# Performance work log

Measured on AMD Instinct MI355X. Metric: run time of the kernel, lower is better.

Reference implementation:

```python
import jax, jax.numpy as jnp
from jax import lax
import numpy as np

GZ = 15.0   # grid extent (float, from gz=15.0)
G = 15      # grid cells per axis


def _disty(p):
    # p: [B, N, 3] points in [0, GZ). 12 features per point:
    # offsets to cell center / lower corner / upper corner (9) + their euclidean norms (3)
    c = jnp.floor(jnp.clip(p, 0.0, GZ - 1e-4))
    off_c = p - (c + 0.5)
    off_l = p - c
    off_u = p - (c + 1.0)
    norms = jnp.stack([jnp.sqrt((o * o).sum(-1)) for o in (off_c, off_l, off_u)], axis=-1)
    return jnp.concatenate([off_c, off_l, off_u, norms], axis=-1)  # [B, N, 12]


def _mlp(x, W1, b1, W2, b2, W3, b3):
    h = jax.nn.elu(x @ W1 + b1)
    h = jax.nn.elu(h @ W2 + b2)
    return h @ W3 + b3  # [B, N, 4]


def _agg(feats, p):
    # scatter-max per-point features into the [G,G,G] grid of each scene
    B, N, C = feats.shape
    cell = jnp.floor(jnp.clip(p, 0.0, GZ - 1e-4)).astype(jnp.int32)  # [B, N, 3]
    flat = (cell[..., 0] * G + cell[..., 1]) * G + cell[..., 2]
    flat = flat + (jnp.arange(B, dtype=jnp.int32) * (G ** 3))[:, None]
    grid = jnp.zeros((B * G ** 3, C), feats.dtype)
    grid = grid.at[flat.reshape(-1)].max(feats.reshape(-1, C))
    return grid.reshape(B, G, G, G, C).transpose(0, 4, 1, 2, 3)  # [B, 4, G, G, G]


def _conv_bn_elu(x, w, b, g, beta, stride):
    y = lax.conv_general_dilated(x, w, (stride,) * 3, [(2, 2)] * 3,
                                 dimension_numbers=('NCDHW', 'OIDHW', 'NCDHW'))
    y = y + b[None, :, None, None, None]
    # BatchNorm3d, training mode (batch statistics), eps=1e-5
    m = y.mean((0, 2, 3, 4), keepdims=True)
    v = ((y - m) ** 2).mean((0, 2, 3, 4), keepdims=True)
    y = (y - m) * lax.rsqrt(v + 1e-5)
    y = y * g[None, :, None, None, None] + beta[None, :, None, None, None]
    return jax.nn.elu(y)


def setup_inputs():
    key = jax.random.key(0)
    ks = jax.random.split(key, 16)
    B, N = 4, 300000
    pts = lambda k: jax.random.uniform(k, (B, N, 3), jnp.float32, 0.0, GZ)
    lin = lambda k, i, o: (jax.random.normal(k, (i, o), jnp.float32) / np.sqrt(i)).astype(jnp.float32)
    inp = {
        'goals': pts(ks[0]), 'inputs': pts(ks[1]), 'backgrounds': pts(ks[2]),
        'W1': lin(ks[3], 12, 16), 'b1': jnp.zeros((16,), jnp.float32),
        'W2': lin(ks[4], 16, 16), 'b2': jnp.zeros((16,), jnp.float32),
        'W3': lin(ks[5], 16, 4),  'b3': jnp.zeros((4,), jnp.float32),
        'conv1_w': (jax.random.normal(ks[6], (8, 12, 5, 5, 5), jnp.float32) / np.sqrt(12 * 125)).astype(jnp.float32),
        'conv1_b': jnp.zeros((8,), jnp.float32),
        'bn1_g': jnp.ones((8,), jnp.float32), 'bn1_b': jnp.zeros((8,), jnp.float32),
        'convs_w': (jax.random.normal(ks[7], (6, 8, 8, 5, 5, 5), jnp.float32) / np.sqrt(8 * 125)).astype(jnp.float32),
        'convs_b': jnp.zeros((6, 8), jnp.float32),
        'bns_g': jnp.ones((6, 8), jnp.float32), 'bns_b': jnp.zeros((6, 8), jnp.float32),
    }
    return inp


def reference(goals, inputs, backgrounds, W1, b1, W2, b2, W3, b3,
              conv1_w, conv1_b, bn1_g, bn1_b, convs_w, convs_b, bns_g, bns_b):
    def encode(p):
        return _agg(_mlp(_disty(p), W1, b1, W2, b2, W3, b3), p)

    scenes = jnp.concatenate([encode(inputs), encode(goals), encode(backgrounds)], axis=1)  # [B,12,G,G,G]
    x = _conv_bn_elu(scenes, conv1_w, conv1_b, bn1_g, bn1_b, 2)  # [B,8,8,8,8]
    for i in range(6):
        x = _conv_bn_elu(x, convs_w[i], convs_b[i], bns_g[i], bns_b[i], 1)
    return x
```

## Files before the change

kernel.cpp:

```cpp
#include <hip/hip_runtime.h>
#include <math.h>

#define B 4
#define NPTS 300000
#define G 15
#define G3 3375
#define PAIR_FLOATS (4*G3)
#define SCENE_FLOATS (B*12*G3)

__device__ __forceinline__ float eluf(float v) {
    return v > 0.0f ? v : __expf(v) - 1.0f;
}

__global__ __launch_bounds__(256)
void mlp_kernel(const float* __restrict__ P0,
                const float* __restrict__ P1,
                const float* __restrict__ P2,
                const float* __restrict__ W1, const float* __restrict__ b1,
                const float* __restrict__ W2, const float* __restrict__ b2,
                const float* __restrict__ W3, const float* __restrict__ b3,
                float4* __restrict__ vals, int* __restrict__ cells,
                int s0, int m)
{
    int b   = blockIdx.y;
    int set = blockIdx.z;
    int i   = blockIdx.x * 256 + threadIdx.x;
    if (i >= m) return;
    const float* P = (set == 0) ? P0 : ((set == 1) ? P1 : P2);

    const float* p = P + ((size_t)b * NPTS + (size_t)(s0 + i)) * 3;
    float px = p[0], py = p[1], pz = p[2];

    const float HI = 14.9999f;
    float cx = floorf(fminf(fmaxf(px, 0.0f), HI));
    float cy = floorf(fminf(fmaxf(py, 0.0f), HI));
    float cz = floorf(fminf(fmaxf(pz, 0.0f), HI));

    float x[12];
    x[0] = px - (cx + 0.5f); x[1] = py - (cy + 0.5f); x[2] = pz - (cz + 0.5f);
    x[3] = px - cx;          x[4] = py - cy;          x[5] = pz - cz;
    x[6] = px - (cx + 1.0f); x[7] = py - (cy + 1.0f); x[8] = pz - (cz + 1.0f);
    x[9]  = sqrtf(x[0]*x[0] + x[1]*x[1] + x[2]*x[2]);
    x[10] = sqrtf(x[3]*x[3] + x[4]*x[4] + x[5]*x[5]);
    x[11] = sqrtf(x[6]*x[6] + x[7]*x[7] + x[8]*x[8]);

    float h1[16];
#pragma unroll
    for (int j = 0; j < 16; ++j) {
        float s = b1[j];
#pragma unroll
        for (int k = 0; k < 12; ++k) s = fmaf(x[k], W1[k*16 + j], s);
        h1[j] = eluf(s);
    }
    float h2[16];
#pragma unroll
    for (int j = 0; j < 16; ++j) {
        float s = b2[j];
#pragma unroll
        for (int k = 0; k < 16; ++k) s = fmaf(h1[k], W2[k*16 + j], s);
        h2[j] = eluf(s);
    }
    float o[4];
#pragma unroll
    for (int j = 0; j < 4; ++j) {
        float s = b3[j];
#pragma unroll
        for (int k = 0; k < 16; ++k) s = fmaf(h2[k], W3[k*4 + j], s);
        o[j] = s;
    }

    int cell = (((int)cx) * G + (int)cy) * G + (int)cz;
    int pair = b * 3 + set;
    vals [(size_t)pair * m + i] = make_float4(o[0], o[1], o[2], o[3]);
    cells[(size_t)pair * m + i] = cell;
}

__global__ __launch_bounds__(256)
void scatter_kernel(const float4* __restrict__ vals,
                    const int* __restrict__ cells,
                    float* __restrict__ scenesR, int K, int m, int carry)
{
    __shared__ unsigned sg[PAIR_FLOATS];

    int rep = blockIdx.x;
    int b   = blockIdx.y;
    int set = blockIdx.z;
    int pair = b * 3 + set;
    float* myrep = scenesR + ((size_t)pair * K + rep) * PAIR_FLOATS;

    if (carry) {
        for (int i = threadIdx.x; i < PAIR_FLOATS; i += 256)
            sg[i] = __float_as_uint(myrep[i]);
    } else {
        for (int i = threadIdx.x; i < PAIR_FLOATS; i += 256)
            sg[i] = 0u;
    }
    __syncthreads();

    int chunk = (m + K - 1) / K;
    int start = rep * chunk;
    int end   = min(m, start + chunk);
    const float4* v = vals  + (size_t)pair * m;
    const int*    c = cells + (size_t)pair * m;

    for (int i = start + (int)threadIdx.x; i < end; i += 256) {
        float4 o = v[i];
        int cell = c[i];
        if (o.x > 0.0f) atomicMax(&sg[          cell], __float_as_uint(o.x));
        if (o.y > 0.0f) atomicMax(&sg[    G3 + cell], __float_as_uint(o.y));
        if (o.z > 0.0f) atomicMax(&sg[2 * G3 + cell], __float_as_uint(o.z));
        if (o.w > 0.0f) atomicMax(&sg[3 * G3 + cell], __float_as_uint(o.w));
    }
    __syncthreads();

    for (int i = threadIdx.x; i < PAIR_FLOATS; i += 256)
        myrep[i] = __uint_as_float(sg[i]);
}

__global__ __launch_bounds__(256)
void reduce_kernel(const float* __restrict__ scenesR, float* __restrict__ scenes,
                   int K)
{
    int t = blockIdx.x * 256 + threadIdx.x;
    if (t >= SCENE_FLOATS) return;
    int pair = t / PAIR_FLOATS;
    int j    = t - pair * PAIR_FLOATS;
    const float* src = scenesR + (size_t)pair * K * PAIR_FLOATS + j;
    float mx = 0.0f;
    for (int r = 0; r < K; ++r)
        mx = fmaxf(mx, src[(size_t)r * PAIR_FLOATS]);
    scenes[t] = mx;
}

__global__ __launch_bounds__(256)
void conv1_kernel(const float* __restrict__ scenes,
                  const float* __restrict__ w,
                  const float* __restrict__ bias,
                  float* __restrict__ y, float* __restrict__ stats)
{
    __shared__ float sred[256];
    int bx = blockIdx.x;
    int od = bx & 7, co = (bx >> 3) & 7, b = bx >> 6;
    int tid = threadIdx.x;
    int ow = tid & 7, oh = (tid >> 3) & 7, ciq = tid >> 6;

    float s = 0.0f;
    for (int cin = 0; cin < 3; ++cin) {
        int ci = ciq * 3 + cin;
        const float* sc = scenes + (size_t)(b * 12 + ci) * G3;
        const float* wc = w + (size_t)(co * 12 + ci) * 125;
#pragma unroll
        for (int kd = 0; kd < 5; ++kd) {
            int id = od * 2 - 2 + kd;
            if ((unsigned)id >= (unsigned)G) continue;
#pragma unroll
            for (int kh = 0; kh < 5; ++kh) {
                int ih = oh * 2 - 2 + kh;
                bool hok = (unsigned)ih < (unsigned)G;
#pragma unroll
                for (int kw = 0; kw < 5; ++kw) {
                    int iw = ow * 2 - 2 + kw;
                    if (hok && (unsigned)iw < (unsigned)G)
                        s = fmaf(sc[(id * G + ih) * G + iw], wc[kd*25 + kh*5 + kw], s);
                }
            }
        }
    }
    sred[tid] = s;
    __syncthreads();
    if (tid < 64) {
        float tot = sred[tid] + sred[64+tid] + sred[128+tid] + sred[192+tid] + bias[co];
        y[(size_t)(b * 8 + co) * 512 + od * 64 + tid] = tot;
        float sum = tot, sq = tot * tot;
#pragma unroll
        for (int o = 32; o > 0; o >>= 1) {
            sum += __shfl_down(sum, o, 64);
            sq  += __shfl_down(sq,  o, 64);
        }
        if (tid == 0) { atomicAdd(&stats[co], sum); atomicAdd(&stats[8 + co], sq); }
    }
}

__global__ __launch_bounds__(256)
void conv_s_kernel(const float* __restrict__ yin,
                   const float* __restrict__ w,
                   const float* __restrict__ bias,
                   const float* __restrict__ g, const float* __restrict__ bet,
                   const float* __restrict__ stats_in,
                   float* __restrict__ yout, float* __restrict__ stats_out)
{
    __shared__ float slab[8 * 5 * 144];
    __shared__ float sscale[8], sshift[8];
    __shared__ float sred[256];

    int bx = blockIdx.x;
    int od = bx & 7, co = (bx >> 3) & 7, b = bx >> 6;
    int tid = threadIdx.x;

    if (tid < 8) {
        float S = stats_in[tid], Q = stats_in[8 + tid];
        float m  = S * (1.0f / 2048.0f);
        float vv = Q * (1.0f / 2048.0f) - m * m;
        float rs = rsqrtf(vv + 1e-5f);
        float sc = g[tid] * rs;
        sscale[tid] = sc;
        sshift[tid] = bet[tid] - m * sc;
    }
    __syncthreads();

    for (int s = tid; s < 5760; s += 256) {
        int ci = s / 720; int r = s % 720;
        int kd = r / 144; int r2 = r % 144;
        int ph = r2 / 12, pw = r2 % 12;
        int id = od - 2 + kd, ih = ph - 2, iw = pw - 2;
        float v = 0.0f;
        if ((unsigned)id < 8u && (unsigned)ih < 8u && (unsigned)iw < 8u) {
            float raw = yin[(size_t)(b * 8 + ci) * 512 + id * 64 + ih * 8 + iw];
            float t = fmaf(raw, sscale[ci], sshift[ci]);
            v = t > 0.0f ? t : __expf(t) - 1.0f;
        }
        slab[s] = v;
    }
    __syncthreads();

    int ow = tid & 7, oh = (tid >> 3) & 7, ciq = tid >> 6;
    float s = 0.0f;
#pragma unroll
    for (int c2 = 0; c2 < 2; ++c2) {
        int ci = ciq * 2 + c2;
        const float* sl = slab + ci * 720;
        const float* wc = w + (size_t)(co * 8 + ci) * 125;
#pragma unroll
        for (int kd = 0; kd < 5; ++kd) {
#pragma unroll
            for (int kh = 0; kh < 5; ++kh) {
                const float* row = sl + kd * 144 + (oh + kh) * 12 + ow;
                const float* wr = wc + kd * 25 + kh * 5;
#pragma unroll
                for (int kw = 0; kw < 5; ++kw) s = fmaf(row[kw], wr[kw], s);
            }
        }
    }
    sred[tid] = s;
    __syncthreads();
    if (tid < 64) {
        float tot = sred[tid] + sred[64+tid] + sred[128+tid] + sred[192+tid] + bias[co];
        yout[(size_t)(b * 8 + co) * 512 + od * 64 + tid] = tot;
        float sum = tot, sq = tot * tot;
#pragma unroll
        for (int o = 32; o > 0; o >>= 1) {
            sum += __shfl_down(sum, o, 64);
            sq  += __shfl_down(sq,  o, 64);
        }
        if (tid == 0) { atomicAdd(&stats_out[co], sum); atomicAdd(&stats_out[8 + co], sq); }
    }
}

__global__ __launch_bounds__(256)
void bn_final_kernel(const float* __restrict__ yin,
                     const float* __restrict__ g, const float* __restrict__ bet,
                     const float* __restrict__ stats_in, float* __restrict__ outp)
{
    int i = blockIdx.x * 256 + threadIdx.x;
    int c = (i >> 9) & 7;
    float S = stats_in[c], Q = stats_in[8 + c];
    float m  = S * (1.0f / 2048.0f);
    float vv = Q * (1.0f / 2048.0f) - m * m;
    float rs = rsqrtf(vv + 1e-5f);
    float sc = g[c] * rs;
    float sh = bet[c] - m * sc;
    float t = fmaf(yin[i], sc, sh);
    outp[i] = t > 0.0f ? t : __expf(t) - 1.0f;
}

extern "C" void kernel_launch(void* const* d_in, const int* in_sizes, int n_in,
                              void* d_out, int out_size, void* d_ws, size_t ws_size,
                              hipStream_t stream)
{
    const float* goals       = (const float*)d_in[0];
    const float* inputs      = (const float*)d_in[1];
    const float* backgrounds = (const float*)d_in[2];
    const float* W1 = (const float*)d_in[3];
    const float* b1 = (const float*)d_in[4];
    const float* W2 = (const float*)d_in[5];
    const float* b2 = (const float*)d_in[6];
    const float* W3 = (const float*)d_in[7];
    const float* b3 = (const float*)d_in[8];
    const float* conv1_w = (const float*)d_in[9];
    const float* conv1_b = (const float*)d_in[10];
    const float* bn1_g   = (const float*)d_in[11];
    const float* bn1_b   = (const float*)d_in[12];
    const float* convs_w = (const float*)d_in[13];
    const float* convs_b = (const float*)d_in[14];
    const float* bns_g   = (const float*)d_in[15];
    const float* bns_b   = (const float*)d_in[16];

    long ws_floats = (long)(ws_size / 4);
    long fixed = SCENE_FLOATS + 2L * 16384 + 112;
    static const int plans[][2] = {
        {42,1},{42,2},{42,4},{24,4},{21,6},{16,8},{8,12},{4,16},{2,32},{1,64}};
    int K = 1, S = 64;
    for (int pi = 0; pi < 10; ++pi) {
        int pk = plans[pi][0], ps = plans[pi][1];
        long mseg = (NPTS + ps - 1) / ps;
        long need = 60L * mseg + (long)pk * SCENE_FLOATS + fixed;
        if (need <= ws_floats) { K = pk; S = ps; break; }
    }
    int Mseg = (NPTS + S - 1) / S;

    float*  wsp     = (float*)d_ws;
    float4* vals    = (float4*)wsp;
    int*    cells   = (int*)(wsp + 48L * Mseg);
    float*  scenesR = wsp + 60L * Mseg;
    float*  scenes  = scenesR + (size_t)K * SCENE_FLOATS;
    float*  yA      = scenes + SCENE_FLOATS;
    float*  yB      = yA + 16384;
    float*  stats   = yB + 16384;

    hipMemsetAsync(stats, 0, 7 * 16 * sizeof(float), stream);

    for (int s = 0; s < S; ++s) {
        int s0 = s * Mseg;
        int m  = min(Mseg, NPTS - s0);
        dim3 agrid((m + 255) / 256, B, 3);
        mlp_kernel<<<agrid, 256, 0, stream>>>(inputs, goals, backgrounds,
                                              W1, b1, W2, b2, W3, b3,
                                              vals, cells, s0, m);
        dim3 bgrid(K, B, 3);
        scatter_kernel<<<bgrid, 256, 0, stream>>>(vals, cells, scenesR, K, m,
                                                  s > 0 ? 1 : 0);
    }

    reduce_kernel<<<(SCENE_FLOATS + 255) / 256, 256, 0, stream>>>(scenesR, scenes, K);

    conv1_kernel<<<256, 256, 0, stream>>>(scenes, conv1_w, conv1_b, yA, stats);

    const float* cur = yA;
    float* nxt = yB;
    for (int i = 0; i < 6; ++i) {
        const float* g   = (i == 0) ? bn1_g : (bns_g + (i - 1) * 8);
        const float* bet = (i == 0) ? bn1_b : (bns_b + (i - 1) * 8);
        conv_s_kernel<<<256, 256, 0, stream>>>(
            cur, convs_w + (size_t)i * 8000, convs_b + i * 8,
            g, bet, stats + i * 16, nxt, stats + (i + 1) * 16);
        const float* tmp = cur; cur = nxt; nxt = (float*)tmp;
    }

    bn_final_kernel<<<64, 256, 0, stream>>>(cur, bns_g + 5 * 8, bns_b + 5 * 8,
                                            stats + 6 * 16, (float*)d_out);
}
```

Measured before the change: 327.4 us.

## Fold stats zeroing into MLP kernel, widen scatter blocks, restructure conv slab fill

Drops the separate memset and has the first MLP block zero the stats buffer instead. Scatter blocks grow from 256 to 512 threads to put more parallelism on the shared-memory atomic max. The conv slab fill now issues coalesced up-front loads of the whole input batch slice and scatters them into a zeroed slab, replacing per-element index math and guarded loads. These are several unrelated micro-changes; the slab change loads more data than needed and adds an extra barrier. The stats zeroing also relies on the first MLP launch running before any conv kernel, and it is repeated on every segment launch.

Result: faster. 301.7 us (-7.8%).

```diff
diff --git a/kernel.cpp b/kernel.cpp
--- a/kernel.cpp
+++ b/kernel.cpp
@@ -20,8 +20,12 @@
                 const float* __restrict__ W2, const float* __restrict__ b2,
                 const float* __restrict__ W3, const float* __restrict__ b3,
                 float4* __restrict__ vals, int* __restrict__ cells,
+                float* __restrict__ stats,
                 int s0, int m)
 {
+    if (blockIdx.x == 0 && blockIdx.y == 0 && blockIdx.z == 0 && threadIdx.x < 128)
+        stats[threadIdx.x] = 0.0f;
+
     int b   = blockIdx.y;
     int set = blockIdx.z;
     int i   = blockIdx.x * 256 + threadIdx.x;
@@ -75,7 +79,7 @@
     cells[(size_t)pair * m + i] = cell;
 }
 
-__global__ __launch_bounds__(256)
+__global__ __launch_bounds__(512)
 void scatter_kernel(const float4* __restrict__ vals,
                     const int* __restrict__ cells,
                     float* __restrict__ scenesR, int K, int m, int carry)
@@ -89,10 +93,10 @@
     float* myrep = scenesR + ((size_t)pair * K + rep) * PAIR_FLOATS;
 
     if (carry) {
-        for (int i = threadIdx.x; i < PAIR_FLOATS; i += 256)
+        for (int i = threadIdx.x; i < PAIR_FLOATS; i += 512)
             sg[i] = __float_as_uint(myrep[i]);
     } else {
-        for (int i = threadIdx.x; i < PAIR_FLOATS; i += 256)
+        for (int i = threadIdx.x; i < PAIR_FLOATS; i += 512)
             sg[i] = 0u;
     }
     __syncthreads();
@@ -103,7 +107,7 @@
     const float4* v = vals  + (size_t)pair * m;
     const int*    c = cells + (size_t)pair * m;
 
-    for (int i = start + (int)threadIdx.x; i < end; i += 256) {
+    for (int i = start + (int)threadIdx.x; i < end; i += 512) {
         float4 o = v[i];
         int cell = c[i];
         if (o.x > 0.0f) atomicMax(&sg[          cell], __float_as_uint(o.x));
@@ -113,7 +117,7 @@
     }
     __syncthreads();
 
-    for (int i = threadIdx.x; i < PAIR_FLOATS; i += 256)
+    for (int i = threadIdx.x; i < PAIR_FLOATS; i += 512)
         myrep[i] = __uint_as_float(sg[i]);
 }
 
@@ -190,15 +194,26 @@
                    float* __restrict__ yout, float* __restrict__ stats_out)
 {
     __shared__ float slab[8 * 5 * 144];
-    __shared__ float sscale[8], sshift[8];
+    __shared__ float sstat[16], sscale[8], sshift[8];
     __shared__ float sred[256];
 
     int bx = blockIdx.x;
     int od = bx & 7, co = (bx >> 3) & 7, b = bx >> 6;
     int tid = threadIdx.x;
 
+    float raw[16];
+#pragma unroll
+    for (int k = 0; k < 16; ++k) {
+        int r = k * 256 + tid;
+        raw[k] = yin[((size_t)(b * 8) << 9) + r];
+    }
+
+    if (tid < 16) sstat[tid] = stats_in[tid];
+    for (int i = tid; i < 5760; i += 256) slab[i] = 0.0f;
+    __syncthreads();
+
     if (tid < 8) {
-        float S = stats_in[tid], Q = stats_in[8 + tid];
+        float S = sstat[tid], Q = sstat[8 + tid];
         float m  = S * (1.0f / 2048.0f);
         float vv = Q * (1.0f / 2048.0f) - m * m;
         float rs = rsqrtf(vv + 1e-5f);
@@ -208,18 +223,17 @@
     }
     __syncthreads();
 
-    for (int s = tid; s < 5760; s += 256) {
-        int ci = s / 720; int r = s % 720;
-        int kd = r / 144; int r2 = r % 144;
-        int ph = r2 / 12, pw = r2 % 12;
-        int id = od - 2 + kd, ih = ph - 2, iw = pw - 2;
-        float v = 0.0f;
-        if ((unsigned)id < 8u && (unsigned)ih < 8u && (unsigned)iw < 8u) {
-            float raw = yin[(size_t)(b * 8 + ci) * 512 + id * 64 + ih * 8 + iw];
-            float t = fmaf(raw, sscale[ci], sshift[ci]);
-            v = t > 0.0f ? t : __expf(t) - 1.0f;
-        }
-        slab[s] = v;
+#pragma unroll
+    for (int k = 0; k < 16; ++k) {
+        int r  = k * 256 + tid;
+        int ci = r >> 9, rem = r & 511;
+        int id = rem >> 6, ih = (rem >> 3) & 7, iw = rem & 7;
+        int kd = id - od + 2;
+        if ((unsigned)kd < 5u) {
+            float t = fmaf(raw[k], sscale[ci], sshift[ci]);
+            slab[ci * 720 + kd * 144 + (ih + 2) * 12 + (iw + 2)] =
+                t > 0.0f ? t : __expf(t) - 1.0f;
+        }
     }
     __syncthreads();
 
@@ -262,6 +276,7 @@
                      const float* __restrict__ stats_in, float* __restrict__ outp)
 {
     int i = blockIdx.x * 256 + threadIdx.x;
+    float v = yin[i];
     int c = (i >> 9) & 7;
     float S = stats_in[c], Q = stats_in[8 + c];
     float m  = S * (1.0f / 2048.0f);
@@ -269,7 +284,7 @@
     float rs = rsqrtf(vv + 1e-5f);
     float sc = g[c] * rs;
     float sh = bet[c] - m * sc;
-    float t = fmaf(yin[i], sc, sh);
+    float t = fmaf(v, sc, sh);
     outp[i] = t > 0.0f ? t : __expf(t) - 1.0f;
 }
 
@@ -296,7 +311,7 @@
     const float* bns_b   = (const float*)d_in[16];
 
     long ws_floats = (long)(ws_size / 4);
-    long fixed = SCENE_FLOATS + 2L * 16384 + 112;
+    long fixed = SCENE_FLOATS + 2L * 16384 + 128;
     static const int plans[][2] = {
         {42,1},{42,2},{42,4},{24,4},{21,6},{16,8},{8,12},{4,16},{2,32},{1,64}};
     int K = 1, S = 64;
@@ -317,17 +332,15 @@
     float*  yB      = yA + 16384;
     float*  stats   = yB + 16384;
 
-    hipMemsetAsync(stats, 0, 7 * 16 * sizeof(float), stream);
-
     for (int s = 0; s < S; ++s) {
         int s0 = s * Mseg;
         int m  = min(Mseg, NPTS - s0);
         dim3 agrid((m + 255) / 256, B, 3);
         mlp_kernel<<<agrid, 256, 0, stream>>>(inputs, goals, backgrounds,
                                               W1, b1, W2, b2, W3, b3,
-                                              vals, cells, s0, m);
+                                              vals, cells, stats, s0, m);
         dim3 bgrid(K, B, 3);
-        scatter_kernel<<<bgrid, 256, 0, stream>>>(vals, cells, scenesR, K, m,
+        scatter_kernel<<<bgrid, 512, 0, stream>>>(vals, cells, scenesR, K, m,
                                                   s > 0 ? 1 : 0);
     }
 
```
